# Kernel optimization log

Measured on AMD Instinct MI355X. Metric: run time of the kernel, lower is better.

## Reference

```python
import jax, jax.numpy as jnp
import numpy as np

B, T, C = 1, 2048, 1024
H, D = 16, 64  # n_head, head_size (n_query_groups == n_head -> plain MHA)


def build_rope_cache(seq_len, n_elem, base=10000):
    theta = 1.0 / (base ** (jnp.arange(0, n_elem, 2, dtype=jnp.float32) / n_elem))
    idx_theta = jnp.outer(jnp.arange(seq_len, dtype=jnp.float32), theta)
    idx_theta = jnp.concatenate([idx_theta, idx_theta], axis=-1)  # torch .repeat(1, 2)
    return jnp.cos(idx_theta), jnp.sin(idx_theta)


def apply_rope(x, cos, sin):
    d = x.shape[-1]
    x1, x2 = x[..., : d // 2], x[..., d // 2 :]
    rotated = jnp.concatenate([-x2, x1], axis=-1)
    return x * cos + rotated * sin


def fastmax_attention(q, k, v):
    """Fastmax: first-order Taylor approx of softmax attention, causal, O(n*d^2).
    score(i,j) = 1 + q_i . k_j (temperature=1, zero RPE, no dropout);
    out_i = sum_{j<=i} score*v_j / sum_{j<=i} score, via causal cumulative sums."""
    n = q.shape[2]
    kcum = jnp.cumsum(k, axis=2)                                       # (B,H,T,D)
    kvcum = jnp.cumsum(jnp.einsum('bhnd,bhne->bhnde', k, v), axis=2)   # (B,H,T,D,D)
    den = jnp.arange(1, n + 1, dtype=q.dtype) + jnp.einsum('bhnd,bhnd->bhn', q, kcum)
    num = jnp.cumsum(v, axis=2) + jnp.einsum('bhnd,bhnde->bhne', q, kvcum)
    return num / den[..., None]


def setup_inputs() -> dict:
    key = jax.random.key(0)
    k1, k2, k3 = jax.random.split(key, 3)
    scale = 0.02
    x = jax.random.normal(k1, (B, T, C), dtype=jnp.float32)
    w_attn = jax.random.normal(k2, (3 * H * D, C), dtype=jnp.float32) * scale
    w_proj = jax.random.normal(k3, (C, H * D), dtype=jnp.float32) * scale
    cos, sin = build_rope_cache(T, D)
    return {"x": x, "w_attn": w_attn, "w_proj": w_proj, "cos": cos, "sin": sin}


def reference(x, w_attn, w_proj, cos, sin):
    Bx, Tx, Cx = x.shape
    qkv = x @ w_attn.T                                  # (B,T,3HD)
    qkv = qkv.reshape(Bx, Tx, H, 3, D).transpose(0, 2, 3, 1, 4)  # (B,H,3,T,D)
    q, k, v = qkv[:, :, 0], qkv[:, :, 1], qkv[:, :, 2]
    q = apply_rope(q, cos, sin)
    k = apply_rope(k, cos, sin)
    y = fastmax_attention(q, k, v)                      # (B,H,T,D)
    y = y.transpose(0, 2, 1, 3).reshape(Bx, Tx, H * D)
    return y @ w_proj.T
```

## Files before the change

kernel.cpp:

```cpp
#include <hip/hip_runtime.h>

#define T_LEN 2048
#define C_DIM 1024
#define H_NUM 16
#define D_DIM 64
#define QKV_N (3 * H_NUM * D_DIM)
#define L_CHK 64
#define NC (T_LEN / L_CHK)

typedef _Float16 h8 __attribute__((ext_vector_type(8)));
typedef _Float16 h4 __attribute__((ext_vector_type(4)));
typedef float f32x4 __attribute__((ext_vector_type(4)));

__global__ __launch_bounds__(256) void split3_f16(
    const float* __restrict__ x, _Float16* __restrict__ xh,
    _Float16* __restrict__ xl, const float* __restrict__ wa,
    _Float16* __restrict__ wah, _Float16* __restrict__ wal,
    const float* __restrict__ wp, _Float16* __restrict__ wph) {
  int i = (blockIdx.x * 256 + threadIdx.x) * 8;
  const float* src;
  _Float16 *dh, *dl = nullptr;
  int base;
  if (i < 2097152) {
    src = x; dh = xh; dl = xl; base = i;
  } else if (i < 2097152 + 3145728) {
    src = wa; dh = wah; dl = wal; base = i - 2097152;
  } else {
    src = wp; dh = wph; base = i - 5242880;
  }
  float4 a = *(const float4*)(src + base);
  float4 b = *(const float4*)(src + base + 4);
  float v[8] = {a.x, a.y, a.z, a.w, b.x, b.y, b.z, b.w};
  h8 hv, lv;
#pragma unroll
  for (int j = 0; j < 8; ++j) {
    float s = v[j] * 64.f;
    _Float16 h = (_Float16)s;
    hv[j] = h;
    lv[j] = (_Float16)(s - (float)h);
  }
  *(h8*)(dh + base) = hv;
  if (dl) *(h8*)(dl + base) = lv;
}

__device__ __forceinline__ void split8(float4 a, float4 b, h8& hi, h8& lo) {
  float v[8] = {a.x, a.y, a.z, a.w, b.x, b.y, b.z, b.w};
#pragma unroll
  for (int m = 0; m < 8; ++m) {
    _Float16 hh = (_Float16)v[m];
    hi[m] = hh;
    lo[m] = (_Float16)(v[m] - (float)hh);
  }
}

template <int BN, bool ROPE, bool SPLIT3>
__global__ __launch_bounds__(256) void gemm_nt_f16(
    const _Float16* __restrict__ Ah, const _Float16* __restrict__ Al,
    const _Float16* __restrict__ Bh, const _Float16* __restrict__ Bl,
    float* __restrict__ C, const float* __restrict__ cosb,
    const float* __restrict__ sinb, _Float16* __restrict__ qh_,
    _Float16* __restrict__ ql_, _Float16* __restrict__ kh_,
    _Float16* __restrict__ kl_, _Float16* __restrict__ kTh_,
    _Float16* __restrict__ kTl_, _Float16* __restrict__ vTh_,
    int M, int N, int K, float outscale) {
  constexpr int NJ = BN / 32;
  constexpr int NARR = SPLIT3 ? 2 : 1;
  constexpr int GEMM_BYTES = (64 * 64 * 2 + BN * 64 * 2) * NARR;
  constexpr int ROPE_BYTES = ROPE ? (2 * 64 * 36 * 4 + 2 * 64 * 64 * 4) : 0;
  constexpr int SMEM_BYTES = GEMM_BYTES > ROPE_BYTES ? GEMM_BYTES : ROPE_BYTES;
  __shared__ __align__(16) char smem[SMEM_BYTES];
  _Float16* sAh = (_Float16*)smem;
  _Float16* sAl = sAh + 64 * 64;
  _Float16* sBh = sAh + 64 * 64 * NARR;
  _Float16* sBl = sBh + BN * 64;
  const int tid = threadIdx.x;
  const int wave = tid >> 6;
  const int lane = tid & 63;
  const int bm = blockIdx.y * 64;
  const int wm = wave >> 1;
  const int wn = wave & 1;
  const int srow = lane >> 3;
  const int sblk = ((lane & 7) ^ srow) * 8;
  const int quad = lane >> 4;
  const int lrow = lane & 15;

  int btype = -1, pi = 0, cb0, cb1;
  if constexpr (ROPE) {
    btype = blockIdx.x >> 3;
    pi = blockIdx.x & 7;
    cb0 = (2 * pi) * 3 + btype;
    cb1 = (2 * pi + 1) * 3 + btype;
  } else {
    cb0 = blockIdx.x * (BN / 64);
    cb1 = cb0 + 1;
  }
  const bool isV = ROPE && (btype == 2);

  f32x4 acc[2][NJ];
#pragma unroll
  for (int i = 0; i < 2; ++i)
#pragma unroll
    for (int j = 0; j < NJ; ++j) acc[i][j] = (f32x4){0.f, 0.f, 0.f, 0.f};

  for (int k0 = 0; k0 < K; k0 += 64) {
#pragma unroll
    for (int it = 0; it < 2; ++it) {
      const int ch = wave + it * 4;
      const int row = ch * 8 + srow;
      const _Float16* ga = Ah + (size_t)(bm + row) * K + k0 + sblk;
      __builtin_amdgcn_global_load_lds(
          (const __attribute__((address_space(1))) void*)ga,
          (__attribute__((address_space(3))) void*)(sAh + ch * 512), 16, 0, 0);
      if constexpr (SPLIT3) {
        if (!isV) {
          const _Float16* gb = Al + (size_t)(bm + row) * K + k0 + sblk;
          __builtin_amdgcn_global_load_lds(
              (const __attribute__((address_space(1))) void*)gb,
              (__attribute__((address_space(3))) void*)(sAl + ch * 512), 16, 0,
              0);
        }
      }
    }
#pragma unroll
    for (int it = 0; it < BN / 32; ++it) {
      const int ch = wave + it * 4;
      const int lr = ch * 8 + srow;
      const int grow = ((lr < 64) ? cb0 : cb1) * 64 + (lr & 63);
      const _Float16* ga = Bh + (size_t)grow * K + k0 + sblk;
      __builtin_amdgcn_global_load_lds(
          (const __attribute__((address_space(1))) void*)ga,
          (__attribute__((address_space(3))) void*)(sBh + ch * 512), 16, 0, 0);
      if constexpr (SPLIT3) {
        if (!isV) {
          const _Float16* gb = Bl + (size_t)grow * K + k0 + sblk;
          __builtin_amdgcn_global_load_lds(
              (const __attribute__((address_space(1))) void*)gb,
              (__attribute__((address_space(3))) void*)(sBl + ch * 512), 16, 0,
              0);
        }
      }
    }
    __syncthreads();
    if (SPLIT3 && !isV) {
#pragma unroll
      for (int kk = 0; kk < 2; ++kk) {
        h8 ah[2], al[2], bh[NJ], bl[NJ];
#pragma unroll
        for (int i = 0; i < 2; ++i) {
          const int row = wm * 32 + i * 16 + lrow;
          const int ra = row * 64 + (((kk * 4 + quad) ^ (row & 7)) * 8);
          ah[i] = *(const h8*)&sAh[ra];
          al[i] = *(const h8*)&sAl[ra];
        }
#pragma unroll
        for (int j = 0; j < NJ; ++j) {
          const int row = wn * (BN / 2) + j * 16 + lrow;
          const int rb = row * 64 + (((kk * 4 + quad) ^ (row & 7)) * 8);
          bh[j] = *(const h8*)&sBh[rb];
          bl[j] = *(const h8*)&sBl[rb];
        }
#pragma unroll
        for (int i = 0; i < 2; ++i)
#pragma unroll
          for (int j = 0; j < NJ; ++j) {
            acc[i][j] = __builtin_amdgcn_mfma_f32_16x16x32_f16(
                ah[i], bh[j], acc[i][j], 0, 0, 0);
            acc[i][j] = __builtin_amdgcn_mfma_f32_16x16x32_f16(
                ah[i], bl[j], acc[i][j], 0, 0, 0);
            acc[i][j] = __builtin_amdgcn_mfma_f32_16x16x32_f16(
                al[i], bh[j], acc[i][j], 0, 0, 0);
          }
      }
    } else {
#pragma unroll
      for (int kk = 0; kk < 2; ++kk) {
        h8 ah[2], bh[NJ];
#pragma unroll
        for (int i = 0; i < 2; ++i) {
          const int row = wm * 32 + i * 16 + lrow;
          const int ra = row * 64 + (((kk * 4 + quad) ^ (row & 7)) * 8);
          ah[i] = *(const h8*)&sAh[ra];
        }
#pragma unroll
        for (int j = 0; j < NJ; ++j) {
          const int row = wn * (BN / 2) + j * 16 + lrow;
          const int rb = row * 64 + (((kk * 4 + quad) ^ (row & 7)) * 8);
          bh[j] = *(const h8*)&sBh[rb];
        }
#pragma unroll
        for (int i = 0; i < 2; ++i)
#pragma unroll
          for (int j = 0; j < NJ; ++j)
            acc[i][j] = __builtin_amdgcn_mfma_f32_16x16x32_f16(
                ah[i], bh[j], acc[i][j], 0, 0, 0);
      }
    }
    __syncthreads();
  }
  if constexpr (!ROPE) {
#pragma unroll
    for (int i = 0; i < 2; ++i) {
      const int rbase = bm + wm * 32 + i * 16 + quad * 4;
#pragma unroll
      for (int j = 0; j < NJ; ++j) {
        const int col = blockIdx.x * BN + wn * (BN / 2) + j * 16 + lrow;
#pragma unroll
        for (int r = 0; r < 4; ++r)
          C[(size_t)(rbase + r) * N + col] = acc[i][j][r] * outscale;
      }
    }
  } else {
    float* cs = (float*)smem;
    float* sn = cs + 2304;
    float* bounce = sn + 2304;
    if (btype < 2) {
      const int el = tid * 8;
      const int t = el >> 5, d0 = el & 31;
      const float* gc = &cosb[(size_t)(bm + t) * D_DIM + d0];
      const float* gs = &sinb[(size_t)(bm + t) * D_DIM + d0];
      *(float4*)&cs[t * 36 + d0] = *(const float4*)gc;
      *(float4*)&cs[t * 36 + d0 + 4] = *(const float4*)(gc + 4);
      *(float4*)&sn[t * 36 + d0] = *(const float4*)gs;
      *(float4*)&sn[t * 36 + d0 + 4] = *(const float4*)(gs + 4);
    }
    __syncthreads();
    const int head = 2 * pi + wn;
    const size_t hb = (size_t)head * T_LEN * D_DIM;
    float fv[2][4][4];
#pragma unroll
    for (int i = 0; i < 2; ++i)
#pragma unroll
      for (int r = 0; r < 4; ++r) {
        const int tloc = wm * 32 + i * 16 + quad * 4 + r;
#pragma unroll
        for (int j = 0; j < 4; ++j) {
          const int d32 = (j & 1) * 16 + lrow;
          float val = acc[i][j][r] * outscale;
          if (btype < 2) {
            float rotv =
                ((j < 2) ? -acc[i][j + 2][r] : acc[i][j - 2][r]) * outscale;
            val = val * cs[tloc * 36 + d32] + rotv * sn[tloc * 36 + d32];
          }
          fv[i][r][j] = val;
        }
      }
    if (btype < 2) {
      _Float16* dh = (btype == 0 ? qh_ : kh_) + hb;
      _Float16* dl = (btype == 0 ? ql_ : kl_) + hb;
#pragma unroll
      for (int i = 0; i < 2; ++i)
#pragma unroll
        for (int r = 0; r < 4; ++r) {
          const size_t trow =
              (size_t)(bm + wm * 32 + i * 16 + quad * 4 + r) * D_DIM;
#pragma unroll
          for (int j = 0; j < 4; ++j) {
            const int d = j * 16 + lrow;
            float f = fv[i][r][j];
            _Float16 hh = (_Float16)f;
            dh[trow + d] = hh;
            dl[trow + d] = (_Float16)(f - (float)hh);
          }
        }
    }
    if (btype >= 1) {
      _Float16* th = (btype == 1 ? kTh_ : vTh_) + hb;
      _Float16* tl = kTl_ + hb;
      float* myb = bounce + wn * 4096;
#pragma unroll
      for (int i = 0; i < 2; ++i)
#pragma unroll
        for (int r = 0; r < 4; ++r) {
          const int tloc = wm * 32 + i * 16 + quad * 4 + r;
#pragma unroll
          for (int j = 0; j < 4; ++j) {
            const int d = j * 16 + lrow;
            myb[tloc * 64 + (d ^ tloc)] = fv[i][r][j];
          }
        }
      __syncthreads();
      const int lt = wm * 64 + lane;
      const int e = lt >> 1;
      const int tg0 = (lt & 1) * 32;
#pragma unroll
      for (int s8 = 0; s8 < 4; ++s8) {
        h8 hv, lv;
#pragma unroll
        for (int s = 0; s < 8; ++s) {
          const int t = tg0 + s8 * 8 + s;
          float f = myb[t * 64 + (e ^ t)];
          _Float16 hh = (_Float16)f;
          hv[s] = hh;
          lv[s] = (_Float16)(f - (float)hh);
        }
        *(h8*)&th[(size_t)e * T_LEN + bm + tg0 + s8 * 8] = hv;
        if (btype == 1)
          *(h8*)&tl[(size_t)e * T_LEN + bm + tg0 + s8 * 8] = lv;
      }
    }
  }
}

__global__ __launch_bounds__(256) void chunk_kvT(
    const _Float16* __restrict__ kTh, const _Float16* __restrict__ kTl,
    const _Float16* __restrict__ vTh, float* __restrict__ kvchunk,
    float* __restrict__ kschunk, float* __restrict__ vschunk) {
  const int blk = blockIdx.x;
  const int h = blk / NC, c = blk % NC;
  const int tid = threadIdx.x;
  const int wave = tid >> 6, lane = tid & 63;
  const int quad = lane >> 4, lrow = lane & 15;
  const size_t hb = (size_t)h * D_DIM * T_LEN;
  const int tb = c * L_CHK;
  h8 avh[2];
  {
    const _Float16* pa = vTh + hb + (size_t)(wave * 16 + lrow) * T_LEN + tb +
                         quad * 8;
    avh[0] = *(const h8*)pa;
    avh[1] = *(const h8*)(pa + 32);
  }
  f32x4 accv[4];
#pragma unroll
  for (int dt = 0; dt < 4; ++dt) accv[dt] = (f32x4){0.f, 0.f, 0.f, 0.f};
#pragma unroll
  for (int dt = 0; dt < 4; ++dt) {
    const _Float16* pb = kTh + hb + (size_t)(dt * 16 + lrow) * T_LEN + tb +
                         quad * 8;
#pragma unroll
    for (int ks = 0; ks < 2; ++ks) {
      h8 bh = *(const h8*)(pb + ks * 32);
      accv[dt] = __builtin_amdgcn_mfma_f32_16x16x32_f16(avh[ks], bh, accv[dt],
                                                        0, 0, 0);
    }
  }
  float* ob = kvchunk + (size_t)blk * (D_DIM * D_DIM);
#pragma unroll
  for (int dt = 0; dt < 4; ++dt)
#pragma unroll
    for (int r = 0; r < 4; ++r)
      ob[(wave * 16 + quad * 4 + r) * D_DIM + dt * 16 + lrow] = accv[dt][r];
  if (tid < 64) {
    const _Float16* p = kTh + hb + (size_t)tid * T_LEN + tb;
    const _Float16* pl = kTl + hb + (size_t)tid * T_LEN + tb;
    float s = 0.f;
#pragma unroll
    for (int i = 0; i < 8; ++i) {
      h8 a = *(const h8*)(p + i * 8), b = *(const h8*)(pl + i * 8);
#pragma unroll
      for (int m = 0; m < 8; ++m) s += (float)a[m] + (float)b[m];
    }
    kschunk[(size_t)blk * D_DIM + tid] = s;
  } else if (tid < 128) {
    const int e = tid - 64;
    const _Float16* p = vTh + hb + (size_t)e * T_LEN + tb;
    float s = 0.f;
#pragma unroll
    for (int i = 0; i < 8; ++i) {
      h8 a = *(const h8*)(p + i * 8);
#pragma unroll
      for (int m = 0; m < 8; ++m) s += (float)a[m];
    }
    vschunk[(size_t)blk * D_DIM + e] = s;
  }
}

__global__ __launch_bounds__(256) void scan_fused(
    const float* __restrict__ kvchunk, _Float16* __restrict__ kvph,
    const float* __restrict__ kschunk, const float* __restrict__ vschunk,
    float* __restrict__ kspref, float* __restrict__ vspref) {
  int b = blockIdx.x;
  int tid = threadIdx.x;
  if (b < 256) {
    int gid = b * 256 + tid;
    int h = gid >> 12;
    int de = gid & 4095;
    float vals[NC];
#pragma unroll
    for (int c = 0; c < NC; ++c)
      vals[c] = kvchunk[((size_t)(h * NC + c) << 12) + de];
    float run = 0.f;
#pragma unroll
    for (int c = 0; c < NC; ++c) {
      kvph[((size_t)(h * NC + c) << 12) + de] = (_Float16)run;
      run += vals[c];
    }
  } else {
    int gid = (b - 256) * 256 + tid;
    int h = gid >> 6, d = gid & 63;
    float kv_[NC], vv_[NC];
#pragma unroll
    for (int c = 0; c < NC; ++c) {
      size_t idx = (size_t)(h * NC + c) * 64 + d;
      kv_[c] = kschunk[idx];
      vv_[c] = vschunk[idx];
    }
    float rk = 0.f, rv = 0.f;
#pragma unroll
    for (int c = 0; c < NC; ++c) {
      size_t idx = (size_t)(h * NC + c) * 64 + d;
      kspref[idx] = rk;
      vspref[idx] = rv;
      rk += kv_[c];
      rv += vv_[c];
    }
  }
}

__global__ __launch_bounds__(256) void attn_mfma(
    const _Float16* __restrict__ qh, const _Float16* __restrict__ ql,
    const _Float16* __restrict__ kh, const _Float16* __restrict__ kl,
    const _Float16* __restrict__ vTh, const _Float16* __restrict__ kvph,
    const float* __restrict__ kspref, const float* __restrict__ vspref,
    _Float16* __restrict__ yh) {
  __shared__ __align__(16) _Float16 sS[2][4][16 * 64];
  const int blk = blockIdx.x;
  const int h = blk / NC, c = blk % NC;
  const int tid = threadIdx.x;
  const int wave = tid >> 6, lane = tid & 63;
  const int quad = lane >> 4, lrow = lane & 15;
  const size_t hb = (size_t)h * T_LEN * D_DIM;
  const size_t hbT = (size_t)h * D_DIM * T_LEN;
  const int t0 = c * L_CHK;
  const f32x4 z4 = {0.f, 0.f, 0.f, 0.f};
  h8 aqh[2], aql[2];
  {
    const _Float16* pq =
        qh + hb + (size_t)(t0 + wave * 16 + lrow) * D_DIM + quad * 8;
    const _Float16* pql =
        ql + hb + (size_t)(t0 + wave * 16 + lrow) * D_DIM + quad * 8;
    aqh[0] = *(const h8*)pq;
    aqh[1] = *(const h8*)(pq + 32);
    aql[0] = *(const h8*)pql;
    aql[1] = *(const h8*)(pql + 32);
  }
  f32x4 sacc[4];
#pragma unroll
  for (int jt = 0; jt < 4; ++jt) sacc[jt] = z4;
#pragma unroll
  for (int jt = 0; jt < 4; ++jt) {
    const _Float16* pk =
        kh + hb + (size_t)(t0 + jt * 16 + lrow) * D_DIM + quad * 8;
    const _Float16* pkl =
        kl + hb + (size_t)(t0 + jt * 16 + lrow) * D_DIM + quad * 8;
#pragma unroll
    for (int ks = 0; ks < 2; ++ks) {
      h8 bh = *(const h8*)(pk + ks * 32);
      h8 bl = *(const h8*)(pkl + ks * 32);
      sacc[jt] = __builtin_amdgcn_mfma_f32_16x16x32_f16(aqh[ks], bh, sacc[jt],
                                                        0, 0, 0);
      sacc[jt] = __builtin_amdgcn_mfma_f32_16x16x32_f16(aqh[ks], bl, sacc[jt],
                                                        0, 0, 0);
      sacc[jt] = __builtin_amdgcn_mfma_f32_16x16x32_f16(aql[ks], bh, sacc[jt],
                                                        0, 0, 0);
    }
  }
  _Float16* shp = &sS[0][wave][0];
  _Float16* slp = &sS[1][wave][0];
#pragma unroll
  for (int jt = 0; jt < 4; ++jt)
#pragma unroll
    for (int r = 0; r < 4; ++r) {
      const int row = quad * 4 + r;
      const int j = jt * 16 + lrow;
      const int rglob = wave * 16 + row;
      float s = (j <= rglob) ? (sacc[jt][r] + 1.f) : 0.f;
      _Float16 hh = (_Float16)s;
      const int adr = row * 64 + ((((j >> 3) ^ (row & 7)) << 3) | (j & 7));
      shp[adr] = hh;
      slp[adr] = (_Float16)(s - (float)hh);
    }
  h8 ash[2], asl[2];
#pragma unroll
  for (int ks = 0; ks < 2; ++ks) {
    const int adr = lrow * 64 + (((ks * 4 + quad) ^ (lrow & 7)) << 3);
    ash[ks] = *(const h8*)&shp[adr];
    asl[ks] = *(const h8*)&slp[adr];
  }
  h8 ones;
#pragma unroll
  for (int m = 0; m < 8; ++m) ones[m] = (_Float16)1.0f;
  f32x4 rs = z4;
#pragma unroll
  for (int ks = 0; ks < 2; ++ks) {
    rs = __builtin_amdgcn_mfma_f32_16x16x32_f16(ash[ks], ones, rs, 0, 0, 0);
    rs = __builtin_amdgcn_mfma_f32_16x16x32_f16(asl[ks], ones, rs, 0, 0, 0);
  }
  f32x4 oacc[4];
#pragma unroll
  for (int et = 0; et < 4; ++et) oacc[et] = z4;
#pragma unroll
  for (int et = 0; et < 4; ++et) {
    const _Float16* pv =
        vTh + hbT + (size_t)(et * 16 + lrow) * T_LEN + t0 + quad * 8;
#pragma unroll
    for (int ks = 0; ks < 2; ++ks) {
      h8 bh = *(const h8*)(pv + ks * 32);
      oacc[et] = __builtin_amdgcn_mfma_f32_16x16x32_f16(ash[ks], bh, oacc[et],
                                                        0, 0, 0);
      oacc[et] = __builtin_amdgcn_mfma_f32_16x16x32_f16(asl[ks], bh, oacc[et],
                                                        0, 0, 0);
    }
  }
  const _Float16* kvp = kvph + ((size_t)blk << 12);
#pragma unroll
  for (int et = 0; et < 4; ++et) {
#pragma unroll
    for (int ks = 0; ks < 2; ++ks) {
      h8 bh = *(const h8*)&kvp[(et * 16 + lrow) * D_DIM + ks * 32 + quad * 8];
      oacc[et] = __builtin_amdgcn_mfma_f32_16x16x32_f16(aqh[ks], bh, oacc[et],
                                                        0, 0, 0);
    }
  }
  const float* ksp = kspref + (size_t)blk * D_DIM;
  f32x4 kacc = z4;
#pragma unroll
  for (int ks = 0; ks < 2; ++ks) {
    const float* pb = ksp + ks * 32 + quad * 8;
    float4 b0 = *(const float4*)pb;
    float4 b1 = *(const float4*)(pb + 4);
    h8 bh, bl;
    split8(b0, b1, bh, bl);
    kacc = __builtin_amdgcn_mfma_f32_16x16x32_f16(aqh[ks], bh, kacc, 0, 0, 0);
    kacc = __builtin_amdgcn_mfma_f32_16x16x32_f16(aqh[ks], bl, kacc, 0, 0, 0);
    kacc = __builtin_amdgcn_mfma_f32_16x16x32_f16(aql[ks], bh, kacc, 0, 0, 0);
  }
  const float* vsp = vspref + (size_t)blk * D_DIM;
#pragma unroll
  for (int r = 0; r < 4; ++r) {
    const int row = wave * 16 + quad * 4 + r;
    const float den = (float)(c * L_CHK) + rs[r] + kacc[r];
    const float inv = 1.f / den;
    const size_t ybase = (size_t)(t0 + row) * (H_NUM * D_DIM) + h * D_DIM;
#pragma unroll
    for (int et = 0; et < 4; ++et) {
      const int e = et * 16 + lrow;
      const float num = oacc[et][r] + vsp[e];
      yh[ybase + e] = (_Float16)(num * inv);
    }
  }
}

extern "C" void kernel_launch(void* const* d_in, const int* in_sizes, int n_in,
                              void* d_out, int out_size, void* d_ws,
                              size_t ws_size, hipStream_t stream) {
  const float* x = (const float*)d_in[0];
  const float* w_attn = (const float*)d_in[1];
  const float* w_proj = (const float*)d_in[2];
  const float* cosb = (const float*)d_in[3];
  const float* sinb = (const float*)d_in[4];
  float* out = (float*)d_out;

  char* ws = (char*)d_ws;
  const size_t MB = 1048576;
  float* kvchunk = (float*)ws;
  _Float16* kvph = (_Float16*)(ws + 8 * MB);
  _Float16* qh = (_Float16*)(ws + 16 * MB);
  _Float16* ql = (_Float16*)(ws + 20 * MB);
  _Float16* kh = (_Float16*)(ws + 24 * MB);
  _Float16* kl = (_Float16*)(ws + 28 * MB);
  _Float16* kTh = (_Float16*)(ws + 32 * MB);
  _Float16* kTl = (_Float16*)(ws + 36 * MB);
  _Float16* vTh = (_Float16*)(ws + 40 * MB);
  _Float16* xh = (_Float16*)(ws + 48 * MB);
  _Float16* xl = (_Float16*)(ws + 52 * MB);
  _Float16* yh = (_Float16*)(ws + 48 * MB);
  _Float16* wah = (_Float16*)(ws + 56 * MB);
  _Float16* wal = (_Float16*)(ws + 62 * MB);
  float* kschunk = (float*)(ws + 56 * MB);
  float* vschunk = (float*)(ws + 56 * MB + 131072);
  float* kspref = (float*)(ws + 56 * MB + 262144);
  float* vspref = (float*)(ws + 56 * MB + 393216);
  _Float16* wph = (_Float16*)(ws + 68 * MB);

  split3_f16<<<3072, 256, 0, stream>>>(x, xh, xl, w_attn, wah, wal, w_proj,
                                       wph);

  {
    dim3 grid(QKV_N / 128, T_LEN / 64);
    gemm_nt_f16<128, true, true><<<grid, 256, 0, stream>>>(
        xh, xl, wah, wal, nullptr, cosb, sinb, qh, ql, kh, kl, kTh, kTl, vTh,
        T_LEN, QKV_N, C_DIM, 1.f / 4096.f);
  }
  chunk_kvT<<<H_NUM * NC, 256, 0, stream>>>(kTh, kTl, vTh, kvchunk, kschunk,
                                            vschunk);
  scan_fused<<<260, 256, 0, stream>>>(kvchunk, kvph, kschunk, vschunk,
                                      kspref, vspref);
  attn_mfma<<<H_NUM * NC, 256, 0, stream>>>(qh, ql, kh, kl, vTh, kvph,
                                            kspref, vspref, yh);
  {
    dim3 grid(C_DIM / 128, T_LEN / 64);
    gemm_nt_f16<128, false, false><<<grid, 256, 0, stream>>>(
        yh, nullptr, wph, nullptr, out, nullptr, nullptr, nullptr, nullptr,
        nullptr, nullptr, nullptr, nullptr, nullptr, T_LEN, C_DIM, C_DIM,
        1.f / 64.f);
  }
}
```

Measured before the change: 159.1 us.

## Fuse chunk-KV, scan and attention kernels with grid barriers; compute chunk sums in GEMM epilogue

Merges the chunk K^T V, prefix-scan and attention kernels into one persistent kernel of 512 blocks that synchronizes with a software global barrier in workspace, which removes two kernel launches and their gaps. Per-chunk sums of k and v are now computed in the QKV GEMM epilogue with wave shuffles, so the low half of transposed k (kTl) is no longer written or read. The output projection GEMM moves to 64-wide N tiles, giving more blocks. The grid barrier assumes all 512 blocks are resident at the same time, which is a deadlock risk. Dropping the low-precision k term may also change the k-sum accuracy.

```diff
diff --git a/kernel.cpp b/kernel.cpp
--- a/kernel.cpp
+++ b/kernel.cpp
@@ -53,6 +53,29 @@
   }
 }
 
+__device__ __forceinline__ void gbar(unsigned* bar, int nb) {
+  __syncthreads();
+  if (threadIdx.x == 0) {
+    __threadfence();
+    unsigned g = __hip_atomic_load(&bar[1], __ATOMIC_RELAXED,
+                                   __HIP_MEMORY_SCOPE_AGENT);
+    unsigned a = __hip_atomic_fetch_add(&bar[0], 1u, __ATOMIC_ACQ_REL,
+                                        __HIP_MEMORY_SCOPE_AGENT);
+    if (a + 1 == (unsigned)nb) {
+      __hip_atomic_store(&bar[0], 0u, __ATOMIC_RELAXED,
+                         __HIP_MEMORY_SCOPE_AGENT);
+      __hip_atomic_fetch_add(&bar[1], 1u, __ATOMIC_RELEASE,
+                             __HIP_MEMORY_SCOPE_AGENT);
+    } else {
+      while (__hip_atomic_load(&bar[1], __ATOMIC_ACQUIRE,
+                               __HIP_MEMORY_SCOPE_AGENT) == g)
+        __builtin_amdgcn_s_sleep(32);
+    }
+    __threadfence();
+  }
+  __syncthreads();
+}
+
 template <int BN, bool ROPE, bool SPLIT3>
 __global__ __launch_bounds__(256) void gemm_nt_f16(
     const _Float16* __restrict__ Ah, const _Float16* __restrict__ Al,
@@ -61,8 +84,8 @@
     const float* __restrict__ sinb, _Float16* __restrict__ qh_,
     _Float16* __restrict__ ql_, _Float16* __restrict__ kh_,
     _Float16* __restrict__ kl_, _Float16* __restrict__ kTh_,
-    _Float16* __restrict__ kTl_, _Float16* __restrict__ vTh_,
-    int M, int N, int K, float outscale) {
+    _Float16* __restrict__ vTh_, float* __restrict__ ksc_,
+    float* __restrict__ vsc_, int M, int N, int K, float outscale) {
   constexpr int NJ = BN / 32;
   constexpr int NARR = SPLIT3 ? 2 : 1;
   constexpr int GEMM_BYTES = (64 * 64 * 2 + BN * 64 * 2) * NARR;
@@ -265,7 +288,6 @@
     }
     if (btype >= 1) {
       _Float16* th = (btype == 1 ? kTh_ : vTh_) + hb;
-      _Float16* tl = kTl_ + hb;
       float* myb = bounce + wn * 4096;
 #pragma unroll
       for (int i = 0; i < 2; ++i)
@@ -278,100 +300,105 @@
             myb[tloc * 64 + (d ^ tloc)] = fv[i][r][j];
           }
         }
+      float ps[4];
+#pragma unroll
+      for (int j = 0; j < 4; ++j) {
+        ps[j] = 0.f;
+#pragma unroll
+        for (int i = 0; i < 2; ++i)
+#pragma unroll
+          for (int r = 0; r < 4; ++r) ps[j] += fv[i][r][j];
+        ps[j] += __shfl_xor(ps[j], 16);
+        ps[j] += __shfl_xor(ps[j], 32);
+      }
       __syncthreads();
-      const int lt = wm * 64 + lane;
-      const int e = lt >> 1;
-      const int tg0 = (lt & 1) * 32;
-#pragma unroll
-      for (int s8 = 0; s8 < 4; ++s8) {
-        h8 hv, lv;
-#pragma unroll
-        for (int s = 0; s < 8; ++s) {
-          const int t = tg0 + s8 * 8 + s;
-          float f = myb[t * 64 + (e ^ t)];
-          _Float16 hh = (_Float16)f;
-          hv[s] = hh;
-          lv[s] = (_Float16)(f - (float)hh);
-        }
-        *(h8*)&th[(size_t)e * T_LEN + bm + tg0 + s8 * 8] = hv;
-        if (btype == 1)
-          *(h8*)&tl[(size_t)e * T_LEN + bm + tg0 + s8 * 8] = lv;
+      {
+        const int lt = wm * 64 + lane;
+        const int e = lt >> 1;
+        const int tg0 = (lt & 1) * 32;
+#pragma unroll
+        for (int s8 = 0; s8 < 4; ++s8) {
+          h8 hv;
+#pragma unroll
+          for (int s = 0; s < 8; ++s) {
+            const int t = tg0 + s8 * 8 + s;
+            hv[s] = (_Float16)myb[t * 64 + (e ^ t)];
+          }
+          *(h8*)&th[(size_t)e * T_LEN + bm + tg0 + s8 * 8] = hv;
+        }
+      }
+      if (quad == 0) {
+#pragma unroll
+        for (int j = 0; j < 4; ++j)
+          cs[(wn * 2 + wm) * 64 + j * 16 + lrow] = ps[j];
+      }
+      __syncthreads();
+      if (wm == 0 && quad == 0) {
+        float* dst = (btype == 1 ? ksc_ : vsc_);
+        const int c = bm >> 6;
+#pragma unroll
+        for (int j = 0; j < 4; ++j) {
+          const int d = j * 16 + lrow;
+          float s = cs[(wn * 2) * 64 + d] + cs[(wn * 2 + 1) * 64 + d];
+          dst[((size_t)head * NC + c) * 64 + d] = s;
+        }
       }
     }
   }
 }
 
-__global__ __launch_bounds__(256) void chunk_kvT(
-    const _Float16* __restrict__ kTh, const _Float16* __restrict__ kTl,
-    const _Float16* __restrict__ vTh, float* __restrict__ kvchunk,
-    float* __restrict__ kschunk, float* __restrict__ vschunk) {
-  const int blk = blockIdx.x;
-  const int h = blk / NC, c = blk % NC;
+__global__ __launch_bounds__(256, 2) void middle_fused(
+    const _Float16* __restrict__ kTh, const _Float16* __restrict__ vTh,
+    float* __restrict__ kvchunk, const float* __restrict__ kschunk,
+    const float* __restrict__ vschunk, _Float16* __restrict__ kvph,
+    float* __restrict__ kspref, float* __restrict__ vspref,
+    const _Float16* __restrict__ qh, const _Float16* __restrict__ ql,
+    const _Float16* __restrict__ kh, const _Float16* __restrict__ kl,
+    _Float16* __restrict__ yh, unsigned* bar) {
+  __shared__ __align__(16) char sm[16384];
   const int tid = threadIdx.x;
+  const int bid = blockIdx.x;
+  const int nb = gridDim.x;
   const int wave = tid >> 6, lane = tid & 63;
   const int quad = lane >> 4, lrow = lane & 15;
-  const size_t hb = (size_t)h * D_DIM * T_LEN;
-  const int tb = c * L_CHK;
-  h8 avh[2];
+  const f32x4 z4 = {0.f, 0.f, 0.f, 0.f};
+
   {
-    const _Float16* pa = vTh + hb + (size_t)(wave * 16 + lrow) * T_LEN + tb +
-                         quad * 8;
-    avh[0] = *(const h8*)pa;
-    avh[1] = *(const h8*)(pa + 32);
-  }
-  f32x4 accv[4];
-#pragma unroll
-  for (int dt = 0; dt < 4; ++dt) accv[dt] = (f32x4){0.f, 0.f, 0.f, 0.f};
-#pragma unroll
-  for (int dt = 0; dt < 4; ++dt) {
-    const _Float16* pb = kTh + hb + (size_t)(dt * 16 + lrow) * T_LEN + tb +
-                         quad * 8;
-#pragma unroll
-    for (int ks = 0; ks < 2; ++ks) {
-      h8 bh = *(const h8*)(pb + ks * 32);
-      accv[dt] = __builtin_amdgcn_mfma_f32_16x16x32_f16(avh[ks], bh, accv[dt],
-                                                        0, 0, 0);
-    }
-  }
-  float* ob = kvchunk + (size_t)blk * (D_DIM * D_DIM);
-#pragma unroll
-  for (int dt = 0; dt < 4; ++dt)
-#pragma unroll
-    for (int r = 0; r < 4; ++r)
-      ob[(wave * 16 + quad * 4 + r) * D_DIM + dt * 16 + lrow] = accv[dt][r];
-  if (tid < 64) {
-    const _Float16* p = kTh + hb + (size_t)tid * T_LEN + tb;
-    const _Float16* pl = kTl + hb + (size_t)tid * T_LEN + tb;
-    float s = 0.f;
-#pragma unroll
-    for (int i = 0; i < 8; ++i) {
-      h8 a = *(const h8*)(p + i * 8), b = *(const h8*)(pl + i * 8);
-#pragma unroll
-      for (int m = 0; m < 8; ++m) s += (float)a[m] + (float)b[m];
-    }
-    kschunk[(size_t)blk * D_DIM + tid] = s;
-  } else if (tid < 128) {
-    const int e = tid - 64;
-    const _Float16* p = vTh + hb + (size_t)e * T_LEN + tb;
-    float s = 0.f;
-#pragma unroll
-    for (int i = 0; i < 8; ++i) {
-      h8 a = *(const h8*)(p + i * 8);
-#pragma unroll
-      for (int m = 0; m < 8; ++m) s += (float)a[m];
-    }
-    vschunk[(size_t)blk * D_DIM + e] = s;
-  }
-}
-
-__global__ __launch_bounds__(256) void scan_fused(
-    const float* __restrict__ kvchunk, _Float16* __restrict__ kvph,
-    const float* __restrict__ kschunk, const float* __restrict__ vschunk,
-    float* __restrict__ kspref, float* __restrict__ vspref) {
-  int b = blockIdx.x;
-  int tid = threadIdx.x;
-  if (b < 256) {
-    int gid = b * 256 + tid;
+    const int h = bid / NC, c = bid % NC;
+    const size_t hbT = (size_t)h * D_DIM * T_LEN;
+    const int tb = c * L_CHK;
+    h8 avh[2];
+    {
+      const _Float16* pa =
+          vTh + hbT + (size_t)(wave * 16 + lrow) * T_LEN + tb + quad * 8;
+      avh[0] = *(const h8*)pa;
+      avh[1] = *(const h8*)(pa + 32);
+    }
+    f32x4 accv[4];
+#pragma unroll
+    for (int dt = 0; dt < 4; ++dt) accv[dt] = z4;
+#pragma unroll
+    for (int dt = 0; dt < 4; ++dt) {
+      const _Float16* pb =
+          kTh + hbT + (size_t)(dt * 16 + lrow) * T_LEN + tb + quad * 8;
+#pragma unroll
+      for (int ks = 0; ks < 2; ++ks) {
+        h8 bh = *(const h8*)(pb + ks * 32);
+        accv[dt] = __builtin_amdgcn_mfma_f32_16x16x32_f16(avh[ks], bh,
+                                                          accv[dt], 0, 0, 0);
+      }
+    }
+    float* ob = kvchunk + (size_t)bid * (D_DIM * D_DIM);
+#pragma unroll
+    for (int dt = 0; dt < 4; ++dt)
+#pragma unroll
+      for (int r = 0; r < 4; ++r)
+        ob[(wave * 16 + quad * 4 + r) * D_DIM + dt * 16 + lrow] = accv[dt][r];
+  }
+  gbar(bar, nb);
+
+  if (bid < 256) {
+    int gid = bid * 256 + tid;
     int h = gid >> 12;
     int de = gid & 4095;
     float vals[NC];
@@ -384,8 +411,8 @@
       kvph[((size_t)(h * NC + c) << 12) + de] = (_Float16)run;
       run += vals[c];
     }
-  } else {
-    int gid = (b - 256) * 256 + tid;
+  } else if (bid < 260) {
+    int gid = (bid - 256) * 256 + tid;
     int h = gid >> 6, d = gid & 63;
     float kv_[NC], vv_[NC];
 #pragma unroll
@@ -404,138 +431,133 @@
       rv += vv_[c];
     }
   }
-}
-
-__global__ __launch_bounds__(256) void attn_mfma(
-    const _Float16* __restrict__ qh, const _Float16* __restrict__ ql,
-    const _Float16* __restrict__ kh, const _Float16* __restrict__ kl,
-    const _Float16* __restrict__ vTh, const _Float16* __restrict__ kvph,
-    const float* __restrict__ kspref, const float* __restrict__ vspref,
-    _Float16* __restrict__ yh) {
-  __shared__ __align__(16) _Float16 sS[2][4][16 * 64];
-  const int blk = blockIdx.x;
-  const int h = blk / NC, c = blk % NC;
-  const int tid = threadIdx.x;
-  const int wave = tid >> 6, lane = tid & 63;
-  const int quad = lane >> 4, lrow = lane & 15;
-  const size_t hb = (size_t)h * T_LEN * D_DIM;
-  const size_t hbT = (size_t)h * D_DIM * T_LEN;
-  const int t0 = c * L_CHK;
-  const f32x4 z4 = {0.f, 0.f, 0.f, 0.f};
-  h8 aqh[2], aql[2];
+  gbar(bar, nb);
+
   {
-    const _Float16* pq =
-        qh + hb + (size_t)(t0 + wave * 16 + lrow) * D_DIM + quad * 8;
-    const _Float16* pql =
-        ql + hb + (size_t)(t0 + wave * 16 + lrow) * D_DIM + quad * 8;
-    aqh[0] = *(const h8*)pq;
-    aqh[1] = *(const h8*)(pq + 32);
-    aql[0] = *(const h8*)pql;
-    aql[1] = *(const h8*)(pql + 32);
-  }
-  f32x4 sacc[4];
-#pragma unroll
-  for (int jt = 0; jt < 4; ++jt) sacc[jt] = z4;
-#pragma unroll
-  for (int jt = 0; jt < 4; ++jt) {
-    const _Float16* pk =
-        kh + hb + (size_t)(t0 + jt * 16 + lrow) * D_DIM + quad * 8;
-    const _Float16* pkl =
-        kl + hb + (size_t)(t0 + jt * 16 + lrow) * D_DIM + quad * 8;
+    const int h = bid / NC, c = bid % NC;
+    const size_t hb = (size_t)h * T_LEN * D_DIM;
+    const size_t hbT = (size_t)h * D_DIM * T_LEN;
+    const int t0 = c * L_CHK;
+    _Float16* sS = (_Float16*)sm;
+    h8 aqh[2], aql[2];
+    {
+      const _Float16* pq =
+          qh + hb + (size_t)(t0 + wave * 16 + lrow) * D_DIM + quad * 8;
+      const _Float16* pql =
+          ql + hb + (size_t)(t0 + wave * 16 + lrow) * D_DIM + quad * 8;
+      aqh[0] = *(const h8*)pq;
+      aqh[1] = *(const h8*)(pq + 32);
+      aql[0] = *(const h8*)pql;
+      aql[1] = *(const h8*)(pql + 32);
+    }
+    f32x4 sacc[4];
+#pragma unroll
+    for (int jt = 0; jt < 4; ++jt) sacc[jt] = z4;
+#pragma unroll
+    for (int jt = 0; jt < 4; ++jt) {
+      const _Float16* pk =
+          kh + hb + (size_t)(t0 + jt * 16 + lrow) * D_DIM + quad * 8;
+      const _Float16* pkl =
+          kl + hb + (size_t)(t0 + jt * 16 + lrow) * D_DIM + quad * 8;
+#pragma unroll
+      for (int ks = 0; ks < 2; ++ks) {
+        h8 bh = *(const h8*)(pk + ks * 32);
+        h8 bl = *(const h8*)(pkl + ks * 32);
+        sacc[jt] = __builtin_amdgcn_mfma_f32_16x16x32_f16(aqh[ks], bh,
+                                                          sacc[jt], 0, 0, 0);
+        sacc[jt] = __builtin_amdgcn_mfma_f32_16x16x32_f16(aqh[ks], bl,
+                                                          sacc[jt], 0, 0, 0);
+        sacc[jt] = __builtin_amdgcn_mfma_f32_16x16x32_f16(aql[ks], bh,
+                                                          sacc[jt], 0, 0, 0);
+      }
+    }
+    _Float16* shp = sS + wave * 1024;
+    _Float16* slp = sS + (4 + wave) * 1024;
+#pragma unroll
+    for (int jt = 0; jt < 4; ++jt)
+#pragma unroll
+      for (int r = 0; r < 4; ++r) {
+        const int row = quad * 4 + r;
+        const int j = jt * 16 + lrow;
+        const int rglob = wave * 16 + row;
+        float s = (j <= rglob) ? (sacc[jt][r] + 1.f) : 0.f;
+        _Float16 hh = (_Float16)s;
+        const int adr = row * 64 + ((((j >> 3) ^ (row & 7)) << 3) | (j & 7));
+        shp[adr] = hh;
+        slp[adr] = (_Float16)(s - (float)hh);
+      }
+    h8 ash[2], asl[2];
 #pragma unroll
     for (int ks = 0; ks < 2; ++ks) {
-      h8 bh = *(const h8*)(pk + ks * 32);
-      h8 bl = *(const h8*)(pkl + ks * 32);
-      sacc[jt] = __builtin_amdgcn_mfma_f32_16x16x32_f16(aqh[ks], bh, sacc[jt],
-                                                        0, 0, 0);
-      sacc[jt] = __builtin_amdgcn_mfma_f32_16x16x32_f16(aqh[ks], bl, sacc[jt],
-                                                        0, 0, 0);
-      sacc[jt] = __builtin_amdgcn_mfma_f32_16x16x32_f16(aql[ks], bh, sacc[jt],
-                                                        0, 0, 0);
-    }
-  }
-  _Float16* shp = &sS[0][wave][0];
-  _Float16* slp = &sS[1][wave][0];
-#pragma unroll
-  for (int jt = 0; jt < 4; ++jt)
+      const int adr = lrow * 64 + (((ks * 4 + quad) ^ (lrow & 7)) << 3);
+      ash[ks] = *(const h8*)&shp[adr];
+      asl[ks] = *(const h8*)&slp[adr];
+    }
+    h8 ones;
+#pragma unroll
+    for (int m = 0; m < 8; ++m) ones[m] = (_Float16)1.0f;
+    f32x4 rs = z4;
+#pragma unroll
+    for (int ks = 0; ks < 2; ++ks) {
+      rs = __builtin_amdgcn_mfma_f32_16x16x32_f16(ash[ks], ones, rs, 0, 0, 0);
+      rs = __builtin_amdgcn_mfma_f32_16x16x32_f16(asl[ks], ones, rs, 0, 0, 0);
+    }
+    f32x4 oacc[4];
+#pragma unroll
+    for (int et = 0; et < 4; ++et) oacc[et] = z4;
+#pragma unroll
+    for (int et = 0; et < 4; ++et) {
+      const _Float16* pv =
+          vTh + hbT + (size_t)(et * 16 + lrow) * T_LEN + t0 + quad * 8;
+#pragma unroll
+      for (int ks = 0; ks < 2; ++ks) {
+        h8 bh = *(const h8*)(pv + ks * 32);
+        oacc[et] = __builtin_amdgcn_mfma_f32_16x16x32_f16(ash[ks], bh,
+                                                          oacc[et], 0, 0, 0);
+        oacc[et] = __builtin_amdgcn_mfma_f32_16x16x32_f16(asl[ks], bh,
+                                                          oacc[et], 0, 0, 0);
+      }
+    }
+    const _Float16* kvp = kvph + ((size_t)bid << 12);
+#pragma unroll
+    for (int et = 0; et < 4; ++et) {
+#pragma unroll
+      for (int ks = 0; ks < 2; ++ks) {
+        h8 bh =
+            *(const h8*)&kvp[(et * 16 + lrow) * D_DIM + ks * 32 + quad * 8];
+        oacc[et] = __builtin_amdgcn_mfma_f32_16x16x32_f16(aqh[ks], bh,
+                                                          oacc[et], 0, 0, 0);
+      }
+    }
+    const float* ksp = kspref + (size_t)bid * D_DIM;
+    f32x4 kacc = z4;
+#pragma unroll
+    for (int ks = 0; ks < 2; ++ks) {
+      const float* pb = ksp + ks * 32 + quad * 8;
+      float4 b0 = *(const float4*)pb;
+      float4 b1 = *(const float4*)(pb + 4);
+      h8 bh, bl;
+      split8(b0, b1, bh, bl);
+      kacc = __builtin_amdgcn_mfma_f32_16x16x32_f16(aqh[ks], bh, kacc, 0, 0,
+                                                    0);
+      kacc = __builtin_amdgcn_mfma_f32_16x16x32_f16(aqh[ks], bl, kacc, 0, 0,
+                                                    0);
+      kacc = __builtin_amdgcn_mfma_f32_16x16x32_f16(aql[ks], bh, kacc, 0, 0,
+                                                    0);
+    }
+    const float* vsp = vspref + (size_t)bid * D_DIM;
 #pragma unroll
     for (int r = 0; r < 4; ++r) {
-      const int row = quad * 4 + r;
-      const int j = jt * 16 + lrow;
-      const int rglob = wave * 16 + row;
-      float s = (j <= rglob) ? (sacc[jt][r] + 1.f) : 0.f;
-      _Float16 hh = (_Float16)s;
-      const int adr = row * 64 + ((((j >> 3) ^ (row & 7)) << 3) | (j & 7));
-      shp[adr] = hh;
-      slp[adr] = (_Float16)(s - (float)hh);
-    }
-  h8 ash[2], asl[2];
-#pragma unroll
-  for (int ks = 0; ks < 2; ++ks) {
-    const int adr = lrow * 64 + (((ks * 4 + quad) ^ (lrow & 7)) << 3);
-    ash[ks] = *(const h8*)&shp[adr];
-    asl[ks] = *(const h8*)&slp[adr];
-  }
-  h8 ones;
-#pragma unroll
-  for (int m = 0; m < 8; ++m) ones[m] = (_Float16)1.0f;
-  f32x4 rs = z4;
-#pragma unroll
-  for (int ks = 0; ks < 2; ++ks) {
-    rs = __builtin_amdgcn_mfma_f32_16x16x32_f16(ash[ks], ones, rs, 0, 0, 0);
-    rs = __builtin_amdgcn_mfma_f32_16x16x32_f16(asl[ks], ones, rs, 0, 0, 0);
-  }
-  f32x4 oacc[4];
-#pragma unroll
-  for (int et = 0; et < 4; ++et) oacc[et] = z4;
-#pragma unroll
-  for (int et = 0; et < 4; ++et) {
-    const _Float16* pv =
-        vTh + hbT + (size_t)(et * 16 + lrow) * T_LEN + t0 + quad * 8;
-#pragma unroll
-    for (int ks = 0; ks < 2; ++ks) {
-      h8 bh = *(const h8*)(pv + ks * 32);
-      oacc[et] = __builtin_amdgcn_mfma_f32_16x16x32_f16(ash[ks], bh, oacc[et],
-                                                        0, 0, 0);
-      oacc[et] = __builtin_amdgcn_mfma_f32_16x16x32_f16(asl[ks], bh, oacc[et],
-                                                        0, 0, 0);
-    }
-  }
-  const _Float16* kvp = kvph + ((size_t)blk << 12);
-#pragma unroll
-  for (int et = 0; et < 4; ++et) {
-#pragma unroll
-    for (int ks = 0; ks < 2; ++ks) {
-      h8 bh = *(const h8*)&kvp[(et * 16 + lrow) * D_DIM + ks * 32 + quad * 8];
-      oacc[et] = __builtin_amdgcn_mfma_f32_16x16x32_f16(aqh[ks], bh, oacc[et],
-                                                        0, 0, 0);
-    }
-  }
-  const float* ksp = kspref + (size_t)blk * D_DIM;
-  f32x4 kacc = z4;
-#pragma unroll
-  for (int ks = 0; ks < 2; ++ks) {
-    const float* pb = ksp + ks * 32 + quad * 8;
-    float4 b0 = *(const float4*)pb;
-    float4 b1 = *(const float4*)(pb + 4);
-    h8 bh, bl;
-    split8(b0, b1, bh, bl);
-    kacc = __builtin_amdgcn_mfma_f32_16x16x32_f16(aqh[ks], bh, kacc, 0, 0, 0);
-    kacc = __builtin_amdgcn_mfma_f32_16x16x32_f16(aqh[ks], bl, kacc, 0, 0, 0);
-    kacc = __builtin_amdgcn_mfma_f32_16x16x32_f16(aql[ks], bh, kacc, 0, 0, 0);
-  }
-  const float* vsp = vspref + (size_t)blk * D_DIM;
-#pragma unroll
-  for (int r = 0; r < 4; ++r) {
-    const int row = wave * 16 + quad * 4 + r;
-    const float den = (float)(c * L_CHK) + rs[r] + kacc[r];
-    const float inv = 1.f / den;
-    const size_t ybase = (size_t)(t0 + row) * (H_NUM * D_DIM) + h * D_DIM;
-#pragma unroll
-    for (int et = 0; et < 4; ++et) {
-      const int e = et * 16 + lrow;
-      const float num = oacc[et][r] + vsp[e];
-      yh[ybase + e] = (_Float16)(num * inv);
+      const int row = wave * 16 + quad * 4 + r;
+      const float den = (float)(c * L_CHK) + rs[r] + kacc[r];
+      const float inv = 1.f / den;
+      const size_t ybase = (size_t)(t0 + row) * (H_NUM * D_DIM) + h * D_DIM;
+#pragma unroll
+      for (int et = 0; et < 4; ++et) {
+        const int e = et * 16 + lrow;
+        const float num = oacc[et][r] + vsp[e];
+        yh[ybase + e] = (_Float16)(num * inv);
+      }
     }
   }
 }
@@ -554,23 +576,25 @@
   const size_t MB = 1048576;
   float* kvchunk = (float*)ws;
   _Float16* kvph = (_Float16*)(ws + 8 * MB);
+  unsigned* bar = (unsigned*)(ws + 12 * MB);
+  float* kschunk = (float*)(ws + 12 * MB + 4096);
+  float* vschunk = (float*)(ws + 12 * MB + 4096 + 131072);
+  float* kspref = (float*)(ws + 12 * MB + 4096 + 262144);
+  float* vspref = (float*)(ws + 12 * MB + 4096 + 393216);
   _Float16* qh = (_Float16*)(ws + 16 * MB);
   _Float16* ql = (_Float16*)(ws + 20 * MB);
   _Float16* kh = (_Float16*)(ws + 24 * MB);
   _Float16* kl = (_Float16*)(ws + 28 * MB);
   _Float16* kTh = (_Float16*)(ws + 32 * MB);
-  _Float16* kTl = (_Float16*)(ws + 36 * MB);
   _Float16* vTh = (_Float16*)(ws + 40 * MB);
   _Float16* xh = (_Float16*)(ws + 48 * MB);
   _Float16* xl = (_Float16*)(ws + 52 * MB);
   _Float16* yh = (_Float16*)(ws + 48 * MB);
   _Float16* wah = (_Float16*)(ws + 56 * MB);
   _Float16* wal = (_Float16*)(ws + 62 * MB);
-  float* kschunk = (float*)(ws + 56 * MB);
-  float* vschunk = (float*)(ws + 56 * MB + 131072);
-  float* kspref = (float*)(ws + 56 * MB + 262144);
-  float* vspref = (float*)(ws + 56 * MB + 393216);
   _Float16* wph = (_Float16*)(ws + 68 * MB);
+
+  hipMemsetAsync(bar, 0, 16, stream);
 
   split3_f16<<<3072, 256, 0, stream>>>(x, xh, xl, w_attn, wah, wal, w_proj,
                                        wph);
@@ -578,20 +602,17 @@
   {
     dim3 grid(QKV_N / 128, T_LEN / 64);
     gemm_nt_f16<128, true, true><<<grid, 256, 0, stream>>>(
-        xh, xl, wah, wal, nullptr, cosb, sinb, qh, ql, kh, kl, kTh, kTl, vTh,
-        T_LEN, QKV_N, C_DIM, 1.f / 4096.f);
-  }
-  chunk_kvT<<<H_NUM * NC, 256, 0, stream>>>(kTh, kTl, vTh, kvchunk, kschunk,
-                                            vschunk);
-  scan_fused<<<260, 256, 0, stream>>>(kvchunk, kvph, kschunk, vschunk,
-                                      kspref, vspref);
-  attn_mfma<<<H_NUM * NC, 256, 0, stream>>>(qh, ql, kh, kl, vTh, kvph,
-                                            kspref, vspref, yh);
+        xh, xl, wah, wal, nullptr, cosb, sinb, qh, ql, kh, kl, kTh, vTh,
+        kschunk, vschunk, T_LEN, QKV_N, C_DIM, 1.f / 4096.f);
+  }
+  middle_fused<<<512, 256, 0, stream>>>(kTh, vTh, kvchunk, kschunk, vschunk,
+                                        kvph, kspref, vspref, qh, ql, kh, kl,
+                                        yh, bar);
   {
-    dim3 grid(C_DIM / 128, T_LEN / 64);
-    gemm_nt_f16<128, false, false><<<grid, 256, 0, stream>>>(
+    dim3 grid(C_DIM / 64, T_LEN / 64);
+    gemm_nt_f16<64, false, false><<<grid, 256, 0, stream>>>(
         yh, nullptr, wph, nullptr, out, nullptr, nullptr, nullptr, nullptr,
-        nullptr, nullptr, nullptr, nullptr, nullptr, T_LEN, C_DIM, C_DIM,
-        1.f / 64.f);
+        nullptr, nullptr, nullptr, nullptr, nullptr, nullptr, T_LEN, C_DIM,
+        C_DIM, 1.f / 64.f);
   }
 }
```

Result: slower. 316.5 us (+98.9%).

## Fuse per-chunk k/v column sums into QKV GEMM epilogue and drop kT low half

Applied to the files above, without the earlier changes.

The QKV GEMM epilogue now reduces its fp32 k and v tile values over each 64-row chunk with shuffles and shared memory, and writes the per-chunk sums directly. This removes the separate re-read of kT high/low and vT in chunk_kvT and removes writing kTl. The sums are now exact fp32 rather than a rebuilt hi+lo value. The output projection GEMM also switches from 128- to 64-wide N tiles, doubling the grid to improve occupancy.

```diff
diff --git a/kernel.cpp b/kernel.cpp
--- a/kernel.cpp
+++ b/kernel.cpp
@@ -61,8 +61,8 @@
     const float* __restrict__ sinb, _Float16* __restrict__ qh_,
     _Float16* __restrict__ ql_, _Float16* __restrict__ kh_,
     _Float16* __restrict__ kl_, _Float16* __restrict__ kTh_,
-    _Float16* __restrict__ kTl_, _Float16* __restrict__ vTh_,
-    int M, int N, int K, float outscale) {
+    _Float16* __restrict__ vTh_, float* __restrict__ ksc_,
+    float* __restrict__ vsc_, int M, int N, int K, float outscale) {
   constexpr int NJ = BN / 32;
   constexpr int NARR = SPLIT3 ? 2 : 1;
   constexpr int GEMM_BYTES = (64 * 64 * 2 + BN * 64 * 2) * NARR;
@@ -265,7 +265,6 @@
     }
     if (btype >= 1) {
       _Float16* th = (btype == 1 ? kTh_ : vTh_) + hb;
-      _Float16* tl = kTl_ + hb;
       float* myb = bounce + wn * 4096;
 #pragma unroll
       for (int i = 0; i < 2; ++i)
@@ -278,44 +277,67 @@
             myb[tloc * 64 + (d ^ tloc)] = fv[i][r][j];
           }
         }
+      float ps[4];
+#pragma unroll
+      for (int j = 0; j < 4; ++j) {
+        ps[j] = 0.f;
+#pragma unroll
+        for (int i = 0; i < 2; ++i)
+#pragma unroll
+          for (int r = 0; r < 4; ++r) ps[j] += fv[i][r][j];
+        ps[j] += __shfl_xor(ps[j], 16);
+        ps[j] += __shfl_xor(ps[j], 32);
+      }
       __syncthreads();
-      const int lt = wm * 64 + lane;
-      const int e = lt >> 1;
-      const int tg0 = (lt & 1) * 32;
-#pragma unroll
-      for (int s8 = 0; s8 < 4; ++s8) {
-        h8 hv, lv;
-#pragma unroll
-        for (int s = 0; s < 8; ++s) {
-          const int t = tg0 + s8 * 8 + s;
-          float f = myb[t * 64 + (e ^ t)];
-          _Float16 hh = (_Float16)f;
-          hv[s] = hh;
-          lv[s] = (_Float16)(f - (float)hh);
-        }
-        *(h8*)&th[(size_t)e * T_LEN + bm + tg0 + s8 * 8] = hv;
-        if (btype == 1)
-          *(h8*)&tl[(size_t)e * T_LEN + bm + tg0 + s8 * 8] = lv;
+      {
+        const int lt = wm * 64 + lane;
+        const int e = lt >> 1;
+        const int tg0 = (lt & 1) * 32;
+#pragma unroll
+        for (int s8 = 0; s8 < 4; ++s8) {
+          h8 hv;
+#pragma unroll
+          for (int s = 0; s < 8; ++s) {
+            const int t = tg0 + s8 * 8 + s;
+            hv[s] = (_Float16)myb[t * 64 + (e ^ t)];
+          }
+          *(h8*)&th[(size_t)e * T_LEN + bm + tg0 + s8 * 8] = hv;
+        }
+      }
+      if (quad == 0) {
+#pragma unroll
+        for (int j = 0; j < 4; ++j)
+          cs[(wn * 2 + wm) * 64 + j * 16 + lrow] = ps[j];
+      }
+      __syncthreads();
+      if (wm == 0 && quad == 0) {
+        float* dst = (btype == 1 ? ksc_ : vsc_);
+        const int c = bm >> 6;
+#pragma unroll
+        for (int j = 0; j < 4; ++j) {
+          const int d = j * 16 + lrow;
+          float s = cs[(wn * 2) * 64 + d] + cs[(wn * 2 + 1) * 64 + d];
+          dst[((size_t)head * NC + c) * 64 + d] = s;
+        }
       }
     }
   }
 }
 
 __global__ __launch_bounds__(256) void chunk_kvT(
-    const _Float16* __restrict__ kTh, const _Float16* __restrict__ kTl,
-    const _Float16* __restrict__ vTh, float* __restrict__ kvchunk,
-    float* __restrict__ kschunk, float* __restrict__ vschunk) {
+    const _Float16* __restrict__ kTh, const _Float16* __restrict__ vTh,
+    float* __restrict__ kvchunk) {
   const int blk = blockIdx.x;
   const int h = blk / NC, c = blk % NC;
   const int tid = threadIdx.x;
   const int wave = tid >> 6, lane = tid & 63;
   const int quad = lane >> 4, lrow = lane & 15;
-  const size_t hb = (size_t)h * D_DIM * T_LEN;
+  const size_t hbT = (size_t)h * D_DIM * T_LEN;
   const int tb = c * L_CHK;
   h8 avh[2];
   {
-    const _Float16* pa = vTh + hb + (size_t)(wave * 16 + lrow) * T_LEN + tb +
-                         quad * 8;
+    const _Float16* pa =
+        vTh + hbT + (size_t)(wave * 16 + lrow) * T_LEN + tb + quad * 8;
     avh[0] = *(const h8*)pa;
     avh[1] = *(const h8*)(pa + 32);
   }
@@ -324,8 +346,8 @@
   for (int dt = 0; dt < 4; ++dt) accv[dt] = (f32x4){0.f, 0.f, 0.f, 0.f};
 #pragma unroll
   for (int dt = 0; dt < 4; ++dt) {
-    const _Float16* pb = kTh + hb + (size_t)(dt * 16 + lrow) * T_LEN + tb +
-                         quad * 8;
+    const _Float16* pb =
+        kTh + hbT + (size_t)(dt * 16 + lrow) * T_LEN + tb + quad * 8;
 #pragma unroll
     for (int ks = 0; ks < 2; ++ks) {
       h8 bh = *(const h8*)(pb + ks * 32);
@@ -339,29 +361,6 @@
 #pragma unroll
     for (int r = 0; r < 4; ++r)
       ob[(wave * 16 + quad * 4 + r) * D_DIM + dt * 16 + lrow] = accv[dt][r];
-  if (tid < 64) {
-    const _Float16* p = kTh + hb + (size_t)tid * T_LEN + tb;
-    const _Float16* pl = kTl + hb + (size_t)tid * T_LEN + tb;
-    float s = 0.f;
-#pragma unroll
-    for (int i = 0; i < 8; ++i) {
-      h8 a = *(const h8*)(p + i * 8), b = *(const h8*)(pl + i * 8);
-#pragma unroll
-      for (int m = 0; m < 8; ++m) s += (float)a[m] + (float)b[m];
-    }
-    kschunk[(size_t)blk * D_DIM + tid] = s;
-  } else if (tid < 128) {
-    const int e = tid - 64;
-    const _Float16* p = vTh + hb + (size_t)e * T_LEN + tb;
-    float s = 0.f;
-#pragma unroll
-    for (int i = 0; i < 8; ++i) {
-      h8 a = *(const h8*)(p + i * 8);
-#pragma unroll
-      for (int m = 0; m < 8; ++m) s += (float)a[m];
-    }
-    vschunk[(size_t)blk * D_DIM + e] = s;
-  }
 }
 
 __global__ __launch_bounds__(256) void scan_fused(
@@ -554,22 +553,21 @@
   const size_t MB = 1048576;
   float* kvchunk = (float*)ws;
   _Float16* kvph = (_Float16*)(ws + 8 * MB);
+  float* kschunk = (float*)(ws + 12 * MB + 4096);
+  float* vschunk = (float*)(ws + 12 * MB + 4096 + 131072);
+  float* kspref = (float*)(ws + 12 * MB + 4096 + 262144);
+  float* vspref = (float*)(ws + 12 * MB + 4096 + 393216);
   _Float16* qh = (_Float16*)(ws + 16 * MB);
   _Float16* ql = (_Float16*)(ws + 20 * MB);
   _Float16* kh = (_Float16*)(ws + 24 * MB);
   _Float16* kl = (_Float16*)(ws + 28 * MB);
   _Float16* kTh = (_Float16*)(ws + 32 * MB);
-  _Float16* kTl = (_Float16*)(ws + 36 * MB);
   _Float16* vTh = (_Float16*)(ws + 40 * MB);
   _Float16* xh = (_Float16*)(ws + 48 * MB);
   _Float16* xl = (_Float16*)(ws + 52 * MB);
   _Float16* yh = (_Float16*)(ws + 48 * MB);
   _Float16* wah = (_Float16*)(ws + 56 * MB);
   _Float16* wal = (_Float16*)(ws + 62 * MB);
-  float* kschunk = (float*)(ws + 56 * MB);
-  float* vschunk = (float*)(ws + 56 * MB + 131072);
-  float* kspref = (float*)(ws + 56 * MB + 262144);
-  float* vspref = (float*)(ws + 56 * MB + 393216);
   _Float16* wph = (_Float16*)(ws + 68 * MB);
 
   split3_f16<<<3072, 256, 0, stream>>>(x, xh, xl, w_attn, wah, wal, w_proj,
@@ -578,20 +576,19 @@
   {
     dim3 grid(QKV_N / 128, T_LEN / 64);
     gemm_nt_f16<128, true, true><<<grid, 256, 0, stream>>>(
-        xh, xl, wah, wal, nullptr, cosb, sinb, qh, ql, kh, kl, kTh, kTl, vTh,
-        T_LEN, QKV_N, C_DIM, 1.f / 4096.f);
-  }
-  chunk_kvT<<<H_NUM * NC, 256, 0, stream>>>(kTh, kTl, vTh, kvchunk, kschunk,
-                                            vschunk);
+        xh, xl, wah, wal, nullptr, cosb, sinb, qh, ql, kh, kl, kTh, vTh,
+        kschunk, vschunk, T_LEN, QKV_N, C_DIM, 1.f / 4096.f);
+  }
+  chunk_kvT<<<H_NUM * NC, 256, 0, stream>>>(kTh, vTh, kvchunk);
   scan_fused<<<260, 256, 0, stream>>>(kvchunk, kvph, kschunk, vschunk,
                                       kspref, vspref);
   attn_mfma<<<H_NUM * NC, 256, 0, stream>>>(qh, ql, kh, kl, vTh, kvph,
                                             kspref, vspref, yh);
   {
-    dim3 grid(C_DIM / 128, T_LEN / 64);
-    gemm_nt_f16<128, false, false><<<grid, 256, 0, stream>>>(
+    dim3 grid(C_DIM / 64, T_LEN / 64);
+    gemm_nt_f16<64, false, false><<<grid, 256, 0, stream>>>(
         yh, nullptr, wph, nullptr, out, nullptr, nullptr, nullptr, nullptr,
-        nullptr, nullptr, nullptr, nullptr, nullptr, T_LEN, C_DIM, C_DIM,
-        1.f / 64.f);
-  }
-}
+        nullptr, nullptr, nullptr, nullptr, nullptr, nullptr, T_LEN, C_DIM,
+        C_DIM, 1.f / 64.f);
+  }
+}
```

After: 151.2 us, median of 2. 5.0% less time.
